# Kernel optimization log

Hardware: AMD Instinct MI355X
Metric: run time of the kernel (lower is better)

## Reference

```python
import jax, jax.numpy as jnp
import numpy as np

GRAY_W = jnp.array([0.2989, 0.587, 0.114], dtype=jnp.float32)  # torchvision rgb_to_grayscale


def bilinear_sample(img, sx, sy):
    """img: [..., H, W]; sx, sy: [Ho, Wo] source pixel coords; zero padding (grid_sample bilinear)."""
    H, W = img.shape[-2], img.shape[-1]
    x0 = jnp.floor(sx)
    y0 = jnp.floor(sy)
    wx1 = sx - x0
    wy1 = sy - y0
    wx0 = 1.0 - wx1
    wy0 = 1.0 - wy1

    def gather(xi, yi):
        valid = (xi >= 0) & (xi <= W - 1) & (yi >= 0) & (yi <= H - 1)
        xc = jnp.clip(xi, 0, W - 1).astype(jnp.int32)
        yc = jnp.clip(yi, 0, H - 1).astype(jnp.int32)
        return img[..., yc, xc] * valid.astype(img.dtype)

    return (gather(x0, y0) * (wy0 * wx0) + gather(x0 + 1.0, y0) * (wy0 * wx1)
            + gather(x0, y0 + 1.0) * (wy1 * wx0) + gather(x0 + 1.0, y0 + 1.0) * (wy1 * wx1))


def forward(adv_patch, lab_batch, img_size):
    B, L = lab_batch.shape[0], lab_batch.shape[1]
    N, S = B * L, img_size
    key = jax.random.key(42)
    kb, kc, ks, kn, ka, ksc, kp = jax.random.split(key, 7)

    # Resize (bilinear, half-pixel centers). All N expanded copies are identical at this
    # point, so resize + color-jitter once on the single patch, then broadcast (same math).
    p = jax.image.resize(adv_patch, (3, S, S), method="bilinear")

    # ColorJitter: one factor per transform per call, applied to the whole batch.
    b = jax.random.uniform(kb, (), minval=0.8, maxval=1.1)
    c = jax.random.uniform(kc, (), minval=0.8, maxval=1.1)
    s = jax.random.uniform(ks, (), minval=0.8, maxval=1.1)
    p = p * b                                                    # brightness
    p = c * p + (1.0 - c) * jnp.einsum('chw,c->hw', p, GRAY_W).mean()   # contrast
    p = s * p + (1.0 - s) * jnp.einsum('chw,c->hw', p, GRAY_W)[None]    # saturation

    # Uniform noise in [-1,1] * noise_factor, per element of the full [N,3,S,S] batch.
    batch = p[None] + 0.15 * jax.random.uniform(kn, (N, 3, S, S), minval=-1.0, maxval=1.0)

    # RandomAffine(degrees=(-45,45), scale=(0.1,0.16)): rotation+scale about image
    # center, one sample per call; inverse map, shared [S,S] grid for all N images.
    theta = jnp.deg2rad(jax.random.uniform(ka, (), minval=-45.0, maxval=45.0))
    sc = jax.random.uniform(ksc, (), minval=0.1, maxval=0.16)
    ctr = (S - 1) / 2.0
    xs = jnp.arange(S, dtype=jnp.float32) - ctr
    dy, dx = jnp.meshgrid(xs, xs, indexing='ij')
    cos_t, sin_t = jnp.cos(theta), jnp.sin(theta)
    sx = (cos_t * dx + sin_t * dy) / sc + ctr
    sy = (-sin_t * dx + cos_t * dy) / sc + ctr
    batch = bilinear_sample(batch, sx, sy)

    # RandomPerspective(distortion_scale=0.6, p=1.0): corners pulled inward by random
    # integer offsets in [0, 0.6*half]; solve homography T with T(endpoint)=startpoint
    # (output->source map), shared for the whole batch.
    dmax = int(0.6 * (S // 2))
    r = jax.random.randint(kp, (8,), 0, dmax + 1).astype(jnp.float32)
    w = jnp.float32(S - 1)
    end = jnp.stack([jnp.stack([r[0], r[1]]),
                     jnp.stack([w - r[2], r[3]]),
                     jnp.stack([w - r[4], w - r[5]]),
                     jnp.stack([r[6], w - r[7]])])  # [4,2] endpoints (tl,tr,br,bl)
    start = jnp.array([[0.0, 0.0], [1.0, 0.0], [1.0, 1.0], [0.0, 1.0]], jnp.float32) * w
    ex, ey = end[:, 0], end[:, 1]
    px, py = start[:, 0], start[:, 1]
    z, o = jnp.zeros(4, jnp.float32), jnp.ones(4, jnp.float32)
    A = jnp.concatenate([
        jnp.stack([ex, ey, o, z, z, z, -px * ex, -px * ey], axis=1),
        jnp.stack([z, z, z, ex, ey, o, -py * ex, -py * ey], axis=1)], axis=0)  # [8,8]
    rhs = jnp.concatenate([px, py])
    h = jnp.linalg.solve(A, rhs)
    xo = jnp.arange(S, dtype=jnp.float32) + 0.5  # torchvision perspective grid offset
    yo_g, xo_g = jnp.meshgrid(xo, xo, indexing='ij')
    den = h[6] * xo_g + h[7] * yo_g + 1.0
    psx = (h[0] * xo_g + h[1] * yo_g + h[2]) / den - 0.5
    psy = (h[3] * xo_g + h[4] * yo_g + h[5]) / den - 0.5
    batch = bilinear_sample(batch, psx, psy)

    return jnp.clip(batch, 0.0, 0.99).reshape(B, L, 3, S, S)


def setup_inputs() -> dict:
    key = jax.random.key(0)
    k1, k2 = jax.random.split(key)
    return {
        "adv_patch": jax.random.uniform(k1, (3, 300, 300), dtype=jnp.float32),
        "lab_batch": jax.random.normal(k2, (8, 14, 5), dtype=jnp.float32),
        "img_size": 416,
    }


def reference(adv_patch, lab_batch, img_size):
    return forward(adv_patch, lab_batch, img_size)
```

## Files before the change

### kernel.cpp

```cpp
#include <hip/hip_runtime.h>
#include <cstdint>
#include <cstring>
#include <cmath>

__host__ __device__ static inline uint32_t rotl32(uint32_t x, int r) {
  return (x << r) | (x >> (32 - r));
}

__host__ __device__ static inline void tf2x32(uint32_t k0, uint32_t k1,
                                              uint32_t c0, uint32_t c1,
                                              uint32_t& o0, uint32_t& o1) {
  const uint32_t ks2 = 0x1BD11BDAu ^ k0 ^ k1;
  uint32_t x0 = c0 + k0;
  uint32_t x1 = c1 + k1;
#define TF_QR(r) { x0 += x1; x1 = rotl32(x1, (r)); x1 ^= x0; }
  TF_QR(13) TF_QR(15) TF_QR(26) TF_QR(6)
  x0 += k1;  x1 += ks2 + 1u;
  TF_QR(17) TF_QR(29) TF_QR(16) TF_QR(24)
  x0 += ks2; x1 += k0 + 2u;
  TF_QR(13) TF_QR(15) TF_QR(26) TF_QR(6)
  x0 += k0;  x1 += k1 + 3u;
  TF_QR(17) TF_QR(29) TF_QR(16) TF_QR(24)
  x0 += k1;  x1 += ks2 + 4u;
  TF_QR(13) TF_QR(15) TF_QR(26) TF_QR(6)
  x0 += ks2; x1 += k0 + 5u;
#undef TF_QR
  o0 = x0; o1 = x1;
}

__host__ __device__ static inline uint32_t tf_bits32(uint32_t k0, uint32_t k1, uint32_t i) {
  uint32_t a, b;
  tf2x32(k0, k1, 0u, i, a, b);
  return a ^ b;
}

__device__ static inline float noise_from_bits(uint32_t bits) {
  uint32_t fb = (bits >> 9) | 0x3f800000u;
  float f = __uint_as_float(fb) - 1.0f;
  float v = f * 2.0f - 1.0f;
  v = fmaxf(-1.0f, v);
  return 0.15f * v;
}

__global__ void __launch_bounds__(256)
k_resize(const float* __restrict__ src, float* __restrict__ p1,
         double* __restrict__ part, float bmul, int S, int inS, int SS) {
  __shared__ double sh[256];
  int t = blockIdx.x * 256 + threadIdx.x;
  double g = 0.0;
  if (t < SS) {
    int y = t / S, x = t - y * S;
    float fs = (float)inS / (float)S;
    float fy = ((float)y + 0.5f) * fs - 0.5f;
    float fx = ((float)x + 0.5f) * fs - 0.5f;
    float y0f = floorf(fy), x0f = floorf(fx);
    float ty = fy - y0f, tx = fx - x0f;
    int y0 = (int)y0f, x0 = (int)x0f;
    int y1 = y0 + 1, x1 = x0 + 1;
    y0 = min(max(y0, 0), inS - 1); y1 = min(max(y1, 0), inS - 1);
    x0 = min(max(x0, 0), inS - 1); x1 = min(max(x1, 0), inS - 1);
    float w00 = (1.f - ty) * (1.f - tx), w01 = (1.f - ty) * tx;
    float w10 = ty * (1.f - tx),         w11 = ty * tx;
    float rgb[3];
    for (int c = 0; c < 3; ++c) {
      const float* pc = src + (size_t)c * inS * inS;
      float v = pc[y0 * inS + x0] * w00 + pc[y0 * inS + x1] * w01 +
                pc[y1 * inS + x0] * w10 + pc[y1 * inS + x1] * w11;
      v *= bmul;
      p1[(size_t)c * SS + t] = v;
      rgb[c] = v;
    }
    g = (double)(0.2989f * rgb[0] + 0.587f * rgb[1] + 0.114f * rgb[2]);
  }
  sh[threadIdx.x] = g;
  __syncthreads();
  for (int s2 = 128; s2 > 0; s2 >>= 1) {
    if (threadIdx.x < s2) sh[threadIdx.x] += sh[threadIdx.x + s2];
    __syncthreads();
  }
  if (threadIdx.x == 0) part[blockIdx.x] = sh[0];
}

__global__ void __launch_bounds__(256)
k_combined(const float* __restrict__ p1, float* __restrict__ b1,
           const double* __restrict__ part, int nb,
           float cc, float ssat,
           uint32_t kn0, uint32_t kn1, int S, int SS, int blo, int bhi, int bw, int bwp,
           float cos_t, float sin_t, float sc, float ctr, int N, int X8,
           int NB1, int NTOT,
           float4* __restrict__ out,
           float h0, float h1, float h2, float h3, float h4, float h5, float h6, float h7) {
  int b = blockIdx.x;
  long long tt = (long long)b * NB1;
  int h_before = (int)(tt / NTOT);
  int h_incl   = (int)((tt + NB1) / NTOT);
  bool is_hash = (h_incl > h_before);

  if (!is_hash) {
    int zb = b - h_before;
    int tid = zb * 256 + threadIdx.x;
    int total = N * S * X8;
    if (tid >= total) return;
    int x8 = tid % X8;
    int t2 = tid / X8;
    int y  = t2 % S;
    int n  = t2 / S;
    float yo  = (float)y + 0.5f;
    float xo0 = (float)(x8 * 8) + 0.5f;
    float xo7 = xo0 + 7.0f;
    float den0 = h6 * xo0 + h7 * yo + 1.0f;
    float den7 = h6 * xo7 + h7 * yo + 1.0f;
    float psx0 = (h0 * xo0 + h1 * yo + h2) / den0 - 0.5f;
    float psy0 = (h3 * xo0 + h4 * yo + h5) / den0 - 0.5f;
    float psx7 = (h0 * xo7 + h1 * yo + h2) / den7 - 0.5f;
    float psy7 = (h3 * xo7 + h4 * yo + h5) / den7 - 0.5f;
    float lox = fminf(psx0, psx7), hix = fmaxf(psx0, psx7);
    float loy = fminf(psy0, psy7), hiy = fmaxf(psy0, psy7);
    float bl = (float)blo - 1.5f, bh = (float)bhi + 1.5f;
    bool exterior = (den0 > 0.0f) && (den7 > 0.0f) &&
                    (hix < bl || lox > bh || hiy < bl || loy > bh);
    if (!exterior) return;
    int X4 = X8 * 2;
    size_t obase = ((size_t)(n * 3) * S + y) * X4 + x8 * 2;
    size_t ostride = (size_t)S * X4;
    float4 z = make_float4(0.f, 0.f, 0.f, 0.f);
#pragma unroll
    for (int c = 0; c < 3; ++c) {
      out[obase + (size_t)c * ostride]     = z;
      out[obase + (size_t)c * ostride + 1] = z;
    }
    return;
  }

  __shared__ double sh[256];
  double a = 0.0;
  for (int i = threadIdx.x; i < nb; i += 256) a += part[i];
  sh[threadIdx.x] = a;
  __syncthreads();
  for (int s2 = 128; s2 > 0; s2 >>= 1) {
    if (threadIdx.x < s2) sh[threadIdx.x] += sh[threadIdx.x + s2];
    __syncthreads();
  }
  float m = (float)(sh[0] / (double)SS);

  int idx = h_before * 256 + threadIdx.x;
  if (idx >= bw * bw * N) return;
  int px = idx % bw;
  int t2 = idx / bw;
  int py = t2 % bw;
  int n  = t2 / bw;

  int xt = blo + px, yt = blo + py;
  float dx = (float)xt - ctr, dy = (float)yt - ctr;
  float sx = (cos_t * dx + sin_t * dy) / sc + ctr;
  float sy = (-sin_t * dx + cos_t * dy) / sc + ctr;
  float x0f = floorf(sx), y0f = floorf(sy);
  float wx1 = sx - x0f, wy1 = sy - y0f;
  float wx0 = 1.f - wx1, wy0 = 1.f - wy1;
  float Wm1 = (float)(S - 1);
  float xtf[4] = {x0f, x0f + 1.f, x0f, x0f + 1.f};
  float ytf[4] = {y0f, y0f, y0f + 1.f, y0f + 1.f};
  float wt[4]  = {wy0 * wx0, wy0 * wx1, wy1 * wx0, wy1 * wx1};
  float acc[3] = {0.f, 0.f, 0.f};
  uint32_t nbase = (uint32_t)(n * 3) * (uint32_t)SS;
  float omc = 1.0f - cc, oms = 1.0f - ssat;
#pragma unroll
  for (int u = 0; u < 4; ++u) {
    bool valid = (xtf[u] >= 0.f) && (xtf[u] <= Wm1) && (ytf[u] >= 0.f) && (ytf[u] <= Wm1);
    if (!valid) continue;
    int ix = (int)xtf[u], iy = (int)ytf[u];
    int sp = iy * S + ix;
    float r = p1[sp], g = p1[SS + sp], bb = p1[2 * SS + sp];
    float r2 = cc * r + omc * m;
    float g2 = cc * g + omc * m;
    float b2 = cc * bb + omc * m;
    float gray = 0.2989f * r2 + 0.587f * g2 + 0.114f * b2;
    float pfv[3];
    pfv[0] = ssat * r2 + oms * gray;
    pfv[1] = ssat * g2 + oms * gray;
    pfv[2] = ssat * b2 + oms * gray;
    uint32_t idx0 = nbase + (uint32_t)sp;
#pragma unroll
    for (int c = 0; c < 3; ++c) {
      uint32_t bits = tf_bits32(kn0, kn1, idx0 + (uint32_t)(c * SS));
      acc[c] += wt[u] * (pfv[c] + noise_from_bits(bits));
    }
  }
#pragma unroll
  for (int c = 0; c < 3; ++c)
    b1[(((size_t)n * 3 + c) * bw + py) * bwp + px] = acc[c];
}

__global__ void __launch_bounds__(256)
k_out_in(const float* __restrict__ b1, float4* __restrict__ out,
         int S, int X8, int blo, int bhi, int bw, int bwp,
         int ylo, int rows, int glo, int gcnt, int total,
         float h0, float h1, float h2, float h3, float h4, float h5, float h6, float h7) {
  int tid = blockIdx.x * 256 + threadIdx.x;
  if (tid >= total) return;
  int x8 = glo + tid % gcnt;
  int t2 = tid / gcnt;
  int y  = ylo + t2 % rows;
  int n  = t2 / rows;

  int X4 = X8 * 2;
  float yo  = (float)y + 0.5f;
  float xo0 = (float)(x8 * 8) + 0.5f;
  float xo7 = xo0 + 7.0f;
  float den0 = h6 * xo0 + h7 * yo + 1.0f;
  float den7 = h6 * xo7 + h7 * yo + 1.0f;
  float psx0 = (h0 * xo0 + h1 * yo + h2) / den0 - 0.5f;
  float psy0 = (h3 * xo0 + h4 * yo + h5) / den0 - 0.5f;
  float psx7 = (h0 * xo7 + h1 * yo + h2) / den7 - 0.5f;
  float psy7 = (h3 * xo7 + h4 * yo + h5) / den7 - 0.5f;
  float lox = fminf(psx0, psx7), hix = fmaxf(psx0, psx7);
  float loy = fminf(psy0, psy7), hiy = fmaxf(psy0, psy7);
  float bl = (float)blo - 1.5f, bh = (float)bhi + 1.5f;
  bool exterior = (den0 > 0.0f) && (den7 > 0.0f) &&
                  (hix < bl || lox > bh || hiy < bl || loy > bh);
  if (exterior) return;

  float acc[3][8];
#pragma unroll
  for (int c = 0; c < 3; ++c)
#pragma unroll
    for (int j = 0; j < 8; ++j) acc[c][j] = 0.f;

  float Wm1 = (float)(S - 1);
#pragma unroll
  for (int j = 0; j < 8; ++j) {
    float xo = (float)(x8 * 8 + j) + 0.5f;
    float den = h6 * xo + h7 * yo + 1.0f;
    float psx = (h0 * xo + h1 * yo + h2) / den - 0.5f;
    float psy = (h3 * xo + h4 * yo + h5) / den - 0.5f;
    float x0f = floorf(psx), y0f = floorf(psy);
    float wx1 = psx - x0f, wy1 = psy - y0f;
    float wx0 = 1.f - wx1, wy0 = 1.f - wy1;
    float xtf[4] = {x0f, x0f + 1.f, x0f, x0f + 1.f};
    float ytf[4] = {y0f, y0f, y0f + 1.f, y0f + 1.f};
    float wt[4]  = {wy0 * wx0, wy0 * wx1, wy1 * wx0, wy1 * wx1};
#pragma unroll
    for (int u = 0; u < 4; ++u) {
      bool valid = (xtf[u] >= 0.f) && (xtf[u] <= Wm1) && (ytf[u] >= 0.f) && (ytf[u] <= Wm1);
      if (!valid) continue;
      int ix = (int)xtf[u] - blo;
      int iy = (int)ytf[u] - blo;
      if (ix < 0 || ix >= bw || iy < 0 || iy >= bw) continue;
#pragma unroll
      for (int c = 0; c < 3; ++c)
        acc[c][j] += wt[u] * b1[(((size_t)n * 3 + c) * bw + iy) * bwp + ix];
    }
  }

  size_t obase = ((size_t)(n * 3) * S + y) * X4 + x8 * 2;
  size_t ostride = (size_t)S * X4;
#pragma unroll
  for (int c = 0; c < 3; ++c) {
    float4 v0, v1;
    v0.x = fminf(fmaxf(acc[c][0], 0.0f), 0.99f);
    v0.y = fminf(fmaxf(acc[c][1], 0.0f), 0.99f);
    v0.z = fminf(fmaxf(acc[c][2], 0.0f), 0.99f);
    v0.w = fminf(fmaxf(acc[c][3], 0.0f), 0.99f);
    v1.x = fminf(fmaxf(acc[c][4], 0.0f), 0.99f);
    v1.y = fminf(fmaxf(acc[c][5], 0.0f), 0.99f);
    v1.z = fminf(fmaxf(acc[c][6], 0.0f), 0.99f);
    v1.w = fminf(fmaxf(acc[c][7], 0.0f), 0.99f);
    out[obase + (size_t)c * ostride]     = v0;
    out[obase + (size_t)c * ostride + 1] = v1;
  }
}

static float bits_to_u01_host(uint32_t bits) {
  uint32_t fb = (bits >> 9) | 0x3f800000u;
  float f;
  std::memcpy(&f, &fb, 4);
  return f - 1.0f;
}

static float host_uniform(uint32_t k0, uint32_t k1, float mn, float mx) {
  uint32_t bits = tf_bits32(k0, k1, 0u);
  float f = bits_to_u01_host(bits);
  float d = mx - mn;
  float t = f * d;
  float v = t + mn;
  return v < mn ? mn : v;
}

static void solve8(float A[8][8], float b[8], float x[8]) {
  for (int k = 0; k < 8; ++k) {
    int piv = k;
    float amax = fabsf(A[k][k]);
    for (int i = k + 1; i < 8; ++i) {
      float v = fabsf(A[i][k]);
      if (v > amax) { amax = v; piv = i; }
    }
    if (piv != k) {
      for (int j = 0; j < 8; ++j) { float t = A[k][j]; A[k][j] = A[piv][j]; A[piv][j] = t; }
      float t = b[k]; b[k] = b[piv]; b[piv] = t;
    }
    for (int i = k + 1; i < 8; ++i) {
      float l = A[i][k] / A[k][k];
      A[i][k] = l;
      for (int j = k + 1; j < 8; ++j) A[i][j] -= l * A[k][j];
      b[i] -= l * b[k];
    }
  }
  for (int i = 7; i >= 0; --i) {
    float s = b[i];
    for (int j = i + 1; j < 8; ++j) s -= A[i][j] * x[j];
    x[i] = s / A[i][i];
  }
}

extern "C" void kernel_launch(void* const* d_in, const int* in_sizes, int n_in,
                              void* d_out, int out_size, void* d_ws, size_t ws_size,
                              hipStream_t stream) {
  const float* adv = (const float*)d_in[0];
  float* out = (float*)d_out;

  int inS = (int)llround(sqrt((double)in_sizes[0] / 3.0));
  int N   = in_sizes[1] / 5;
  if (N <= 0) N = 112;
  int S   = (int)llround(sqrt((double)out_size / (3.0 * N)));
  int SS  = S * S;

  uint32_t K[7][2];
  for (int i = 0; i < 7; ++i)
    tf2x32(0u, 42u, 0u, (uint32_t)i, K[i][0], K[i][1]);

  float bmul = host_uniform(K[0][0], K[0][1], 0.8f, 1.1f);
  float cc   = host_uniform(K[1][0], K[1][1], 0.8f, 1.1f);
  float ssat = host_uniform(K[2][0], K[2][1], 0.8f, 1.1f);
  float adeg = host_uniform(K[4][0], K[4][1], -45.f, 45.f);
  float theta = adeg * (float)(M_PI / 180.0);
  float sc   = host_uniform(K[5][0], K[5][1], 0.1f, 0.16f);
  float cos_t = cosf(theta), sin_t = sinf(theta);

  int dmax = (int)(0.6 * (double)(S / 2));
  uint32_t span = (uint32_t)(dmax + 1);
  uint32_t mult = ((65536u % span) * (65536u % span)) % span;
  uint32_t kp1[2], kp2[2];
  tf2x32(K[6][0], K[6][1], 0u, 0u, kp1[0], kp1[1]);
  tf2x32(K[6][0], K[6][1], 0u, 1u, kp2[0], kp2[1]);
  float r[8];
  for (int i = 0; i < 8; ++i) {
    uint32_t hi = tf_bits32(kp1[0], kp1[1], (uint32_t)i);
    uint32_t lo = tf_bits32(kp2[0], kp2[1], (uint32_t)i);
    uint32_t v = ((hi % span) * mult + (lo % span)) % span;
    r[i] = (float)v;
  }

  float w = (float)(S - 1);
  float ex[4] = {r[0], w - r[2], w - r[4], r[6]};
  float ey[4] = {r[1], r[3], w - r[5], w - r[7]};
  float px4[4] = {0.f, w, w, 0.f};
  float py4[4] = {0.f, 0.f, w, w};
  float A[8][8];
  float rhs[8];
  for (int i = 0; i < 4; ++i) {
    A[i][0] = ex[i]; A[i][1] = ey[i]; A[i][2] = 1.f;
    A[i][3] = 0.f;   A[i][4] = 0.f;   A[i][5] = 0.f;
    A[i][6] = -px4[i] * ex[i]; A[i][7] = -px4[i] * ey[i];
    rhs[i] = px4[i];
    A[4 + i][0] = 0.f; A[4 + i][1] = 0.f; A[4 + i][2] = 0.f;
    A[4 + i][3] = ex[i]; A[4 + i][4] = ey[i]; A[4 + i][5] = 1.f;
    A[4 + i][6] = -py4[i] * ex[i]; A[4 + i][7] = -py4[i] * ey[i];
    rhs[4 + i] = py4[i];
  }
  float h[8];
  solve8(A, rhs, h);

  float ctr = (float)(S - 1) * 0.5f;
  float a_half = (ctr + 2.0f) * sc;
  float bbh = a_half * (fabsf(cos_t) + fabsf(sin_t)) + 3.0f;
  int blo = (int)floorf(ctr - bbh); if (blo < 0) blo = 0;
  int bhi = (int)ceilf(ctr + bbh);  if (bhi > S - 1) bhi = S - 1;
  int bw = bhi - blo + 1;
  int bwp = (bw + 15) & ~15;

  int X8 = S / 8;
  int ylo = S, yhi = -1, glo = X8, ghi = -1;
  {
    double H0 = h[0], H1 = h[1], H2 = h[2], H3 = h[3], H4 = h[4], H5 = h[5], H6 = h[6], H7 = h[7];
    double bl = (double)blo - 3.0, bh = (double)bhi + 3.0;
    for (int y = 0; y < S; ++y) {
      double yo = y + 0.5;
      for (int g = 0; g < X8; ++g) {
        double xo0 = g * 8 + 0.5, xo7 = xo0 + 7.0;
        double den0 = H6 * xo0 + H7 * yo + 1.0;
        double den7 = H6 * xo7 + H7 * yo + 1.0;
        bool ext;
        if (den0 > 0.0 && den7 > 0.0) {
          double psx0 = (H0 * xo0 + H1 * yo + H2) / den0 - 0.5;
          double psy0 = (H3 * xo0 + H4 * yo + H5) / den0 - 0.5;
          double psx7 = (H0 * xo7 + H1 * yo + H2) / den7 - 0.5;
          double psy7 = (H3 * xo7 + H4 * yo + H5) / den7 - 0.5;
          double lox = fmin(psx0, psx7), hix = fmax(psx0, psx7);
          double loy = fmin(psy0, psy7), hiy = fmax(psy0, psy7);
          ext = (hix < bl || lox > bh || hiy < bl || loy > bh);
        } else {
          ext = false;
        }
        if (!ext) {
          if (y < ylo) ylo = y;
          if (y > yhi) yhi = y;
          if (g < glo) glo = g;
          if (g > ghi) ghi = g;
        }
      }
    }
  }
  int rows = (yhi >= ylo) ? (yhi - ylo + 1) : 0;
  int gcnt = (ghi >= glo) ? (ghi - glo + 1) : 0;

  size_t psize = (size_t)SS * 3 * sizeof(float);
  float*  p1   = (float*)d_ws;
  double* part = (double*)((char*)d_ws + psize);
  float*  b1   = (float*)((char*)d_ws + psize + 8192);

  int nb = (SS + 255) / 256;

  k_resize<<<nb, 256, 0, stream>>>(adv, p1, part, bmul, S, inS, SS);

  int NZ  = (N * S * X8 + 255) / 256;
  int NB1 = (bw * bw * N + 255) / 256;
  int NTOT = NZ + NB1;
  k_combined<<<NTOT, 256, 0, stream>>>(
      p1, b1, part, nb, cc, ssat,
      K[3][0], K[3][1], S, SS, blo, bhi, bw, bwp,
      cos_t, sin_t, sc, ctr, N, X8, NB1, NTOT, (float4*)out,
      h[0], h[1], h[2], h[3], h[4], h[5], h[6], h[7]);

  if (rows > 0 && gcnt > 0) {
    int total = N * rows * gcnt;
    k_out_in<<<(total + 255) / 256, 256, 0, stream>>>(
        b1, (float4*)out, S, X8, blo, bhi, bw, bwp,
        ylo, rows, glo, gcnt, total,
        h[0], h[1], h[2], h[3], h[4], h[5], h[6], h[7]);
  }
}
```

Measured before the change: 76.02 us.

## Split exterior zero-fill blocks across all three kernels to balance work

The zero-fill of exterior output tiles, which previously ran entirely inside the combined kernel, is now split across the resize, combined and interior-output kernels (roughly 29/42/29 of the blocks). The aim is to give the light resize and interior kernels memory-store work so the device stays busy, instead of leaving the combined kernel with one large zero-fill tail. The cost is extra branching in each kernel and a fixed split ratio that may not match the real per-kernel load. The interior kernel is now always launched even when it has no interior work.

```diff
diff --git a/kernel.cpp b/kernel.cpp
--- a/kernel.cpp
+++ b/kernel.cpp
@@ -42,9 +42,53 @@
   return 0.15f * v;
 }
 
+__device__ static inline void zero_role(int g, int Gtot, int N, int S, int X8,
+                                        int blo, int bhi, float4* __restrict__ out,
+                                        float h0, float h1, float h2, float h3,
+                                        float h4, float h5, float h6, float h7) {
+  if (g >= Gtot) return;
+  int x8 = g % X8;
+  int t2 = g / X8;
+  int y  = t2 % S;
+  int n  = t2 / S;
+  float yo  = (float)y + 0.5f;
+  float xo0 = (float)(x8 * 8) + 0.5f;
+  float xo7 = xo0 + 7.0f;
+  float den0 = h6 * xo0 + h7 * yo + 1.0f;
+  float den7 = h6 * xo7 + h7 * yo + 1.0f;
+  float psx0 = (h0 * xo0 + h1 * yo + h2) / den0 - 0.5f;
+  float psy0 = (h3 * xo0 + h4 * yo + h5) / den0 - 0.5f;
+  float psx7 = (h0 * xo7 + h1 * yo + h2) / den7 - 0.5f;
+  float psy7 = (h3 * xo7 + h4 * yo + h5) / den7 - 0.5f;
+  float lox = fminf(psx0, psx7), hix = fmaxf(psx0, psx7);
+  float loy = fminf(psy0, psy7), hiy = fmaxf(psy0, psy7);
+  float bl = (float)blo - 1.5f, bh = (float)bhi + 1.5f;
+  bool exterior = (den0 > 0.0f) && (den7 > 0.0f) &&
+                  (hix < bl || lox > bh || hiy < bl || loy > bh);
+  if (!exterior) return;
+  int X4 = X8 * 2;
+  size_t obase = ((size_t)(n * 3) * S + y) * X4 + x8 * 2;
+  size_t ostride = (size_t)S * X4;
+  float4 z = make_float4(0.f, 0.f, 0.f, 0.f);
+  out[obase]                = z;
+  out[obase + 1]            = z;
+  out[obase + ostride]      = z;
+  out[obase + ostride + 1]  = z;
+  out[obase + 2 * ostride]     = z;
+  out[obase + 2 * ostride + 1] = z;
+}
+
 __global__ void __launch_bounds__(256)
-k_resize(const float* __restrict__ src, float* __restrict__ p1,
-         double* __restrict__ part, float bmul, int S, int inS, int SS) {
+k_resize_z(const float* __restrict__ src, float* __restrict__ p1,
+           double* __restrict__ part, float bmul, int S, int inS, int SS, int nbA,
+           int zstart, int Gtot, int N, int X8, int blo, int bhi,
+           float4* __restrict__ out,
+           float h0, float h1, float h2, float h3, float h4, float h5, float h6, float h7) {
+  if ((int)blockIdx.x >= nbA) {
+    int g = zstart + ((int)blockIdx.x - nbA) * 256 + (int)threadIdx.x;
+    zero_role(g, Gtot, N, S, X8, blo, bhi, out, h0, h1, h2, h3, h4, h5, h6, h7);
+    return;
+  }
   __shared__ double sh[256];
   int t = blockIdx.x * 256 + threadIdx.x;
   double g = 0.0;
@@ -87,7 +131,7 @@
            float cc, float ssat,
            uint32_t kn0, uint32_t kn1, int S, int SS, int blo, int bhi, int bw, int bwp,
            float cos_t, float sin_t, float sc, float ctr, int N, int X8,
-           int NB1, int NTOT,
+           int NB1, int NTOT, int zstart, int Gtot,
            float4* __restrict__ out,
            float h0, float h1, float h2, float h3, float h4, float h5, float h6, float h7) {
   int b = blockIdx.x;
@@ -98,37 +142,8 @@
 
   if (!is_hash) {
     int zb = b - h_before;
-    int tid = zb * 256 + threadIdx.x;
-    int total = N * S * X8;
-    if (tid >= total) return;
-    int x8 = tid % X8;
-    int t2 = tid / X8;
-    int y  = t2 % S;
-    int n  = t2 / S;
-    float yo  = (float)y + 0.5f;
-    float xo0 = (float)(x8 * 8) + 0.5f;
-    float xo7 = xo0 + 7.0f;
-    float den0 = h6 * xo0 + h7 * yo + 1.0f;
-    float den7 = h6 * xo7 + h7 * yo + 1.0f;
-    float psx0 = (h0 * xo0 + h1 * yo + h2) / den0 - 0.5f;
-    float psy0 = (h3 * xo0 + h4 * yo + h5) / den0 - 0.5f;
-    float psx7 = (h0 * xo7 + h1 * yo + h2) / den7 - 0.5f;
-    float psy7 = (h3 * xo7 + h4 * yo + h5) / den7 - 0.5f;
-    float lox = fminf(psx0, psx7), hix = fmaxf(psx0, psx7);
-    float loy = fminf(psy0, psy7), hiy = fmaxf(psy0, psy7);
-    float bl = (float)blo - 1.5f, bh = (float)bhi + 1.5f;
-    bool exterior = (den0 > 0.0f) && (den7 > 0.0f) &&
-                    (hix < bl || lox > bh || hiy < bl || loy > bh);
-    if (!exterior) return;
-    int X4 = X8 * 2;
-    size_t obase = ((size_t)(n * 3) * S + y) * X4 + x8 * 2;
-    size_t ostride = (size_t)S * X4;
-    float4 z = make_float4(0.f, 0.f, 0.f, 0.f);
-#pragma unroll
-    for (int c = 0; c < 3; ++c) {
-      out[obase + (size_t)c * ostride]     = z;
-      out[obase + (size_t)c * ostride + 1] = z;
-    }
+    int g = zstart + zb * 256 + (int)threadIdx.x;
+    zero_role(g, Gtot, N, S, X8, blo, bhi, out, h0, h1, h2, h3, h4, h5, h6, h7);
     return;
   }
 
@@ -192,12 +207,18 @@
 }
 
 __global__ void __launch_bounds__(256)
-k_out_in(const float* __restrict__ b1, float4* __restrict__ out,
-         int S, int X8, int blo, int bhi, int bw, int bwp,
-         int ylo, int rows, int glo, int gcnt, int total,
-         float h0, float h1, float h2, float h3, float h4, float h5, float h6, float h7) {
+k_out_in_z(const float* __restrict__ b1, float4* __restrict__ out,
+           int S, int X8, int blo, int bhi, int bw, int bwp,
+           int ylo, int rows, int glo, int gcnt, int totalInt, int nbInt,
+           int zstart, int Gtot, int N,
+           float h0, float h1, float h2, float h3, float h4, float h5, float h6, float h7) {
+  if ((int)blockIdx.x >= nbInt) {
+    int g = zstart + ((int)blockIdx.x - nbInt) * 256 + (int)threadIdx.x;
+    zero_role(g, Gtot, N, S, X8, blo, bhi, out, h0, h1, h2, h3, h4, h5, h6, h7);
+    return;
+  }
   int tid = blockIdx.x * 256 + threadIdx.x;
-  if (tid >= total) return;
+  if (tid >= totalInt) return;
   int x8 = glo + tid % gcnt;
   int t2 = tid / gcnt;
   int y  = ylo + t2 % rows;
@@ -418,24 +439,36 @@
   double* part = (double*)((char*)d_ws + psize);
   float*  b1   = (float*)((char*)d_ws + psize + 8192);
 
-  int nb = (SS + 255) / 256;
-
-  k_resize<<<nb, 256, 0, stream>>>(adv, p1, part, bmul, S, inS, SS);
-
-  int NZ  = (N * S * X8 + 255) / 256;
-  int NB1 = (bw * bw * N + 255) / 256;
-  int NTOT = NZ + NB1;
+  int nbA = (SS + 255) / 256;
+
+  int Gtot = N * S * X8;
+  int NZ   = (Gtot + 255) / 256;
+  int NB1  = (bw * bw * N + 255) / 256;
+  int ZB   = (int)((long long)NZ * 42 / 100);
+  int ZA   = (NZ - ZB) / 2;
+  int ZC   = NZ - ZB - ZA;
+  int zA0  = 0;
+  int zB0  = ZA * 256;
+  int zC0  = (ZA + ZB) * 256;
+
+  k_resize_z<<<nbA + ZA, 256, 0, stream>>>(
+      adv, p1, part, bmul, S, inS, SS, nbA,
+      zA0, Gtot, N, X8, blo, bhi, (float4*)out,
+      h[0], h[1], h[2], h[3], h[4], h[5], h[6], h[7]);
+
+  int NTOT = NB1 + ZB;
   k_combined<<<NTOT, 256, 0, stream>>>(
-      p1, b1, part, nb, cc, ssat,
+      p1, b1, part, nbA, cc, ssat,
       K[3][0], K[3][1], S, SS, blo, bhi, bw, bwp,
-      cos_t, sin_t, sc, ctr, N, X8, NB1, NTOT, (float4*)out,
+      cos_t, sin_t, sc, ctr, N, X8, NB1, NTOT, zB0, Gtot, (float4*)out,
       h[0], h[1], h[2], h[3], h[4], h[5], h[6], h[7]);
 
-  if (rows > 0 && gcnt > 0) {
-    int total = N * rows * gcnt;
-    k_out_in<<<(total + 255) / 256, 256, 0, stream>>>(
-        b1, (float4*)out, S, X8, blo, bhi, bw, bwp,
-        ylo, rows, glo, gcnt, total,
-        h[0], h[1], h[2], h[3], h[4], h[5], h[6], h[7]);
-  }
-}
+  int totalInt = N * rows * gcnt;
+  int nbInt = (totalInt + 255) / 256;
+  if (totalInt <= 0) nbInt = 0;
+  k_out_in_z<<<nbInt + ZC, 256, 0, stream>>>(
+      b1, (float4*)out, S, X8, blo, bhi, bw, bwp,
+      ylo, rows, glo, gcnt, totalInt, nbInt,
+      zC0, Gtot, N,
+      h[0], h[1], h[2], h[3], h[4], h[5], h[6], h[7]);
+}
```

New measurement: 77.09 us. No clear change (+1.4%).
